# Optimization experiments

Hardware: AMD Instinct MI355X
Metric: run time of the kernel (lower is better)

## Reference

```python
import jax, jax.numpy as jnp
import numpy as np

B, N, D, H = 16, 256, 128, 8
HD = D // H
PAIR_DIMS = [64, 64, 64]
EPS = 1e-8


def _pairwise_lv_fts(x):
    # x: [B, 4, N] four-vectors (px, py, pz, E); returns [B, N, N, 4] = (lnkt, lnz, lndelta, lnm2)
    px, py, pz, e = x[:, 0], x[:, 1], x[:, 2], x[:, 3]
    pt = jnp.sqrt(jnp.clip(px ** 2 + py ** 2, EPS))          # [B, N]
    rap = 0.5 * jnp.log1p(2.0 * pz / jnp.clip(e - pz, 1e-20))
    phi = jnp.arctan2(py, px)
    d_rap = rap[:, :, None] - rap[:, None, :]                 # [B, N, N]
    d_phi = (phi[:, :, None] - phi[:, None, :] + np.pi) % (2.0 * np.pi) - np.pi
    delta = jnp.sqrt(d_rap ** 2 + d_phi ** 2)
    lndelta = jnp.log(jnp.clip(delta, EPS))
    ptmin = jnp.minimum(pt[:, :, None], pt[:, None, :])
    lnkt = jnp.log(jnp.clip(ptmin * delta, EPS))
    lnz = jnp.log(jnp.clip(ptmin / jnp.clip(pt[:, :, None] + pt[:, None, :], EPS), EPS))
    es = e[:, :, None] + e[:, None, :]
    pxs = px[:, :, None] + px[:, None, :]
    pys = py[:, :, None] + py[:, None, :]
    pzs = pz[:, :, None] + pz[:, None, :]
    lnm2 = jnp.log(jnp.clip(es ** 2 - pxs ** 2 - pys ** 2 - pzs ** 2, EPS))
    return jnp.stack([lnkt, lnz, lndelta, lnm2], axis=-1)


def setup_inputs() -> dict:
    key = jax.random.key(0)
    ks = jax.random.split(key, 12)
    p3 = jax.random.normal(ks[0], (B, 3, N), jnp.float32)
    e = jnp.sqrt((p3 ** 2).sum(1, keepdims=True)
                 + jnp.abs(jax.random.normal(ks[1], (B, 1, N), jnp.float32)) ** 2 + 0.1)
    x_pf = jnp.concatenate([p3, e], axis=1)                   # physical four-vectors [B,4,N]
    x_feat = jax.random.normal(ks[2], (B, N, D), jnp.float32) * 0.02
    dims = [4] + PAIR_DIMS + [H]
    pw = {}
    for i in range(4):
        pw[f"pair_w{i}"] = jax.random.normal(ks[3 + i], (dims[i], dims[i + 1]), jnp.float32) / np.sqrt(dims[i])
        pw[f"pair_b{i}"] = jnp.zeros((dims[i + 1],), jnp.float32)
    proj = {n: jax.random.normal(k, (D, D), jnp.float32) / np.sqrt(D)
            for n, k in zip(["wq", "wk", "wv", "wo"], jax.random.split(ks[7], 4))}
    bias = {n: jnp.zeros((D,), jnp.float32) for n in ["bq", "bk", "bv", "bo"]}
    return dict(x_pf=x_pf, x_feat=x_feat, **pw, **proj, **bias)


def reference(x_pf, x_feat, pair_w0, pair_b0, pair_w1, pair_b1, pair_w2, pair_b2,
              pair_w3, pair_b3, wq, wk, wv, wo, bq, bk, bv, bo):
    # pairwise Lorentz-invariant features -> dense attention bias
    u = _pairwise_lv_fts(x_pf)                                # [B, N, N, 4]
    for w, b in ((pair_w0, pair_b0), (pair_w1, pair_b1), (pair_w2, pair_b2)):
        u = jax.nn.gelu(u @ w + b)
    attn_bias = jnp.transpose(u @ pair_w3 + pair_b3, (0, 3, 1, 2))  # [B, H, N, N]
    # multi-head attention with pairwise bias
    q = (x_feat @ wq + bq).reshape(B, N, H, HD)
    k = (x_feat @ wk + bk).reshape(B, N, H, HD)
    v = (x_feat @ wv + bv).reshape(B, N, H, HD)
    scores = jnp.einsum("bihd,bjhd->bhij", q, k) / np.sqrt(HD) + attn_bias
    attn = jax.nn.softmax(scores, axis=-1)
    out = jnp.einsum("bhij,bjhd->bihd", attn, v).reshape(B, N, D)
    return out @ wo + bo                                      # [B, N, D]
```

## Files before the change

kernel.cpp:

```cpp
#include <hip/hip_runtime.h>
#include <hip/hip_bf16.h>
#include <math.h>

#define B_ 16
#define N_ 256
#define D_ 128
#define H_ 8
#define HD_ 16
#define EPS_ 1e-8f
#define PI_F 3.14159265358979323846f
#define TWO_PI_F 6.28318530717958647692f
#define INV_TWO_PI_F 0.15915494309189533577f
#define L2E_F 1.4426950408889634f

#define OFF_PT   0
#define OFF_RAP  4096
#define OFF_PHI  8192
#define OFF_PX   12288
#define OFF_PY   16384
#define OFF_PZ   20480
#define OFF_E    24576
#define OFF_Q    28672
#define OFF_BIAS (28672 + 3*524288)
#define OFF_AO   (OFF_BIAS + 8388608)
#define OFF_WPACK (OFF_AO + 524288)

#define UA0  0
#define UA1H 2048
#define UA1L 6144
#define UA2H 10240
#define UA2L 14336
#define UA3H 18432
#define UA3L 19456
#define UQKV 20480

typedef _Float16 f16x8 __attribute__((ext_vector_type(8)));
typedef _Float16 f16x4 __attribute__((ext_vector_type(4)));
typedef _Float16 f16x2 __attribute__((ext_vector_type(2)));
typedef __attribute__((ext_vector_type(4))) float f4;
typedef __attribute__((ext_vector_type(4))) unsigned int u4;

__device__ __forceinline__ unsigned pkh2(float a, float b) {
    f16x2 v = { (_Float16)a, (_Float16)b };
    return __builtin_bit_cast(unsigned, v);
}
__device__ __forceinline__ float f16res(float x) {
    return x - (float)(_Float16)x;
}

__device__ __forceinline__ float gelu_f(float x) {
    float y2 = x * fmaf(0.10294337f, x * x, 2.3022079f);
    float e = __builtin_amdgcn_exp2f(-y2);
    return x * __builtin_amdgcn_rcpf(1.0f + e);
}


__global__ __launch_bounds__(256) void k_prep(
    const float* __restrict__ w0, const float* __restrict__ w1,
    const float* __restrict__ w2, const float* __restrict__ w3,
    const float* __restrict__ wq, const float* __restrict__ wk,
    const float* __restrict__ wv, const float* __restrict__ wo,
    const float* __restrict__ x_pf,
    _Float16* __restrict__ wp, float* __restrict__ ws) {
    if (blockIdx.x >= 64) {
        int idx = (blockIdx.x - 64) * 256 + threadIdx.x;
        int b = idx >> 8, n = idx & 255;
        const float* base = x_pf + (size_t)b * 4 * N_;
        float px = base[0 * N_ + n];
        float py = base[1 * N_ + n];
        float pz = base[2 * N_ + n];
        float e  = base[3 * N_ + n];
        float pt  = sqrtf(fmaxf(px * px + py * py, EPS_));
        float rap = 0.5f * log1pf(2.0f * pz / fmaxf(e - pz, 1e-20f));
        float phi = atan2f(py, px);
        ws[OFF_PT  + idx] = pt;
        ws[OFF_RAP + idx] = rap;
        ws[OFF_PHI + idx] = phi;
        ws[OFF_PX  + idx] = px;
        ws[OFF_PY  + idx] = py;
        ws[OFF_PZ  + idx] = pz;
        ws[OFF_E   + idx] = e;
        return;
    }
    int id0 = blockIdx.x * 256 + threadIdx.x;
    const int gs = 64 * 256;
    for (int e = id0; e < 2048; e += gs) {
        int fi = e >> 3, j = e & 7;
        int mt = fi >> 6, lane = fi & 63;
        int q = lane >> 4, ln = lane & 15;
        int m = mt * 16 + ln;
        _Float16 v = (_Float16)0.0f;
        if (q == 0) v = (j < 4) ? (_Float16)w0[j * 64 + m]
                                : (_Float16)f16res(w0[(j - 4) * 64 + m]);
        else if (q == 1) v = (j < 4) ? (_Float16)w0[j * 64 + m] : (_Float16)0.0f;
        wp[UA0 + e] = v;
    }
    for (int e = id0; e < 4096; e += gs) {
        int fi = e >> 3, j = e & 7;
        int mt = fi >> 7, ks = (fi >> 6) & 1, lane = fi & 63;
        int q = lane >> 4;
        int m = mt * 16 + (lane & 15);
        int k = (2 * (j >> 2) + ks) * 16 + q * 4 + (j & 3);
        float x1 = w1[k * 64 + m];
        wp[UA1H + e] = (_Float16)x1;
        wp[UA1L + e] = (_Float16)f16res(x1);
        float x2 = w2[k * 64 + m];
        wp[UA2H + e] = (_Float16)x2;
        wp[UA2L + e] = (_Float16)f16res(x2);
    }
    for (int e = id0; e < 1024; e += gs) {
        int fi = e >> 3, j = e & 7;
        int ks = fi >> 6, lane = fi & 63;
        int q = lane >> 4;
        int m = lane & 15;
        int k = (2 * (j >> 2) + ks) * 16 + q * 4 + (j & 3);
        float x = (m < 8) ? w3[k * 8 + m] : 0.0f;
        wp[UA3H + e] = (_Float16)x;
        wp[UA3L + e] = (_Float16)f16res(x);
    }
    const float* mats[4] = { wq, wk, wv, wo };
#pragma unroll 1
    for (int mi = 0; mi < 4; ++mi) {
        const float* W = mats[mi];
        _Float16* dst = wp + UQKV + mi * 32768;
        for (int e = id0; e < 16384; e += gs) {
            int fi = e >> 3, j = e & 7;
            int mt = fi >> 8, ks = (fi >> 6) & 3, lane = fi & 63;
            int k = ks * 32 + ((lane >> 4) << 3) + j;
            int o = mt * 16 + (lane & 15);
            float x = W[k * 128 + o];
            dst[e] = (_Float16)x;
            dst[16384 + e] = (_Float16)f16res(x);
        }
    }
}

__device__ __forceinline__ void epi_frag(const f4 (&acc)[4][4], const float* __restrict__ bg,
                                         int q, u4 (&Bu)[4][2]) {
#pragma unroll
    for (int mt = 0; mt < 4; ++mt) {
        f4 bv = *(const f4*)&bg[mt * 16 + q * 4];
        int ks = mt & 1, hi = (mt >> 1) * 2;
#pragma unroll
        for (int nt = 0; nt < 4; ++nt) {
            float g0 = gelu_f(acc[mt][nt][0] + bv[0]);
            float g1 = gelu_f(acc[mt][nt][1] + bv[1]);
            float g2 = gelu_f(acc[mt][nt][2] + bv[2]);
            float g3 = gelu_f(acc[mt][nt][3] + bv[3]);
            Bu[nt][ks][hi]     = pkh2(g0, g1);
            Bu[nt][ks][hi + 1] = pkh2(g2, g3);
        }
    }
}

__device__ __forceinline__ void mid_layer(f4 (&acc)[4][4],
                                          const _Float16* __restrict__ wh,
                                          const _Float16* __restrict__ wl,
                                          int lane, const u4 (&Bu)[4][2]) {
    const f4 zero4 = { 0.f, 0.f, 0.f, 0.f };
#pragma unroll
    for (int mt = 0; mt < 4; ++mt) {
        f16x8 ah0 = *(const f16x8*)&wh[((mt * 2 + 0) * 64 + lane) * 8];
        f16x8 ah1 = *(const f16x8*)&wh[((mt * 2 + 1) * 64 + lane) * 8];
        f16x8 al0 = *(const f16x8*)&wl[((mt * 2 + 0) * 64 + lane) * 8];
        f16x8 al1 = *(const f16x8*)&wl[((mt * 2 + 1) * 64 + lane) * 8];
#pragma unroll
        for (int nt = 0; nt < 4; ++nt) {
            f16x8 b0 = __builtin_bit_cast(f16x8, Bu[nt][0]);
            f16x8 b1 = __builtin_bit_cast(f16x8, Bu[nt][1]);
            f4 c = zero4;
            c = __builtin_amdgcn_mfma_f32_16x16x32_f16(ah0, b0, c, 0, 0, 0);
            c = __builtin_amdgcn_mfma_f32_16x16x32_f16(al0, b0, c, 0, 0, 0);
            c = __builtin_amdgcn_mfma_f32_16x16x32_f16(ah1, b1, c, 0, 0, 0);
            c = __builtin_amdgcn_mfma_f32_16x16x32_f16(al1, b1, c, 0, 0, 0);
            acc[mt][nt] = c;
        }
    }
}

__device__ __forceinline__ void mfma_core64x16(
    const float* __restrict__ xrow, const _Float16* __restrict__ wpm,
    int mtbase, const float* __restrict__ biasv, int lane, f4 (&cc)[4]) {
    int q = lane >> 4;
    const f4 zero4 = { 0.f, 0.f, 0.f, 0.f };
    f16x8 Bh[4], Bl[4];
#pragma unroll
    for (int ks = 0; ks < 4; ++ks) {
        const float* p = xrow + ks * 32 + q * 8;
        float4 xa = ((const float4*)p)[0];
        float4 xb = ((const float4*)p)[1];
        u4 hu = { pkh2(xa.x, xa.y), pkh2(xa.z, xa.w), pkh2(xb.x, xb.y), pkh2(xb.z, xb.w) };
        u4 lu = { pkh2(f16res(xa.x), f16res(xa.y)), pkh2(f16res(xa.z), f16res(xa.w)),
                  pkh2(f16res(xb.x), f16res(xb.y)), pkh2(f16res(xb.z), f16res(xb.w)) };
        Bh[ks] = __builtin_bit_cast(f16x8, hu);
        Bl[ks] = __builtin_bit_cast(f16x8, lu);
    }
#pragma unroll
    for (int mtl = 0; mtl < 4; ++mtl) {
        int mt = mtbase + mtl;
        f4 c = zero4;
#pragma unroll
        for (int ks = 0; ks < 4; ++ks) {
            const _Float16* fa = wpm + ((size_t)((mt * 4 + ks) * 64 + lane)) * 8;
            f16x8 ah = *(const f16x8*)fa;
            f16x8 al = *(const f16x8*)(fa + 16384);
            c = __builtin_amdgcn_mfma_f32_16x16x32_f16(ah, Bh[ks], c, 0, 0, 0);
            c = __builtin_amdgcn_mfma_f32_16x16x32_f16(ah, Bl[ks], c, 0, 0, 0);
            c = __builtin_amdgcn_mfma_f32_16x16x32_f16(al, Bh[ks], c, 0, 0, 0);
        }
        f4 bv = *(const f4*)&biasv[mtl * 16 + q * 4];
        cc[mtl] = c + bv;
    }
}

__global__ __launch_bounds__(256, 4) void k_pair_qkv(
    const float* __restrict__ ws, const _Float16* __restrict__ wp,
    const float* __restrict__ b0g, const float* __restrict__ b1g,
    const float* __restrict__ b2g, const float* __restrict__ b3g,
    float* __restrict__ bias_out,
    const float* __restrict__ xf,
    const float* __restrict__ bqv, const float* __restrict__ bkv, const float* __restrict__ bvv,
    _Float16* __restrict__ qh, _Float16* __restrict__ kh,
    _Float16* __restrict__ kl, _Float16* __restrict__ vh) {
    int tid = threadIdx.x;
    int lane = tid & 63;
    int ln = lane & 15, q = lane >> 4;

    if (blockIdx.x < 384) {
        int wid = blockIdx.x * 4 + (tid >> 6);
        int og = wid % 6, tg = wid / 6;
        int mi = og >> 1, ch = og & 1;
        const _Float16* wpm = wp + UQKV + mi * 32768;
        const float* bias = (mi == 0) ? bqv : ((mi == 1) ? bkv : bvv);
        size_t tok = (size_t)(tg * 16 + ln);
        f4 cc[4];
        mfma_core64x16(xf + tok * 128, wpm, ch * 4, bias + ch * 64, lane, cc);
        _Float16* hout = (mi == 0) ? qh : ((mi == 1) ? kh : vh);
        int b = (int)(tok >> 8), tl = (int)(tok & 255);
#pragma unroll
        for (int mtl = 0; mtl < 4; ++mtl) {
            int head = ch * 4 + mtl;
            size_t off = ((size_t)((b * 8 + head) * 256 + tl)) * 16 + q * 4;
            f16x4 hv;
#pragma unroll
            for (int r = 0; r < 4; ++r) hv[r] = (_Float16)cc[mtl][r];
            *(f16x4*)&hout[off] = hv;
            if (mi == 1) {
                f16x4 lv;
#pragma unroll
                for (int r = 0; r < 4; ++r) lv[r] = (_Float16)(cc[mtl][r] - (float)hv[r]);
                *(f16x4*)&kl[off] = lv;
            }
        }
        return;
    }

    int w2 = (blockIdx.x - 384) * 4 + (tid >> 6);
    int b = w2 / 640;
    int w = w2 - b * 640;
    int it, rr, nj;
    if (w < 256)      { it = 0; rr = w;       nj = 4; }
    else if (w < 448) { it = 1; rr = w - 256; nj = 3; }
    else if (w < 576) { it = 2; rr = w - 448; nj = 2; }
    else              { it = 3; rr = w - 576; nj = 1; }
    int i  = it * 64 + rr / nj;
    int jt = it + rr % nj;
    int j0 = jt * 64;
    int row = (b << 8) + i;

    unsigned FH01, FH23, FL01, FL23;
    {
        int ib = row;
        int jb = (b << 8) + j0 + lane;
        float pt_i = ws[OFF_PT + ib],  rap_i = ws[OFF_RAP + ib], phi_i = ws[OFF_PHI + ib];
        float px_i = ws[OFF_PX + ib],  py_i  = ws[OFF_PY  + ib];
        float pz_i = ws[OFF_PZ + ib],  e_i   = ws[OFF_E   + ib];
        float pt_j = ws[OFF_PT + jb],  rap_j = ws[OFF_RAP + jb], phi_j = ws[OFF_PHI + jb];
        float px_j = ws[OFF_PX + jb],  py_j  = ws[OFF_PY  + jb];
        float pz_j = ws[OFF_PZ + jb],  e_j   = ws[OFF_E   + jb];

        float drap = rap_i - rap_j;
        float xw = phi_i - phi_j + PI_F;
        float mw = xw - TWO_PI_F * floorf(xw * INV_TWO_PI_F);
        float dphi = mw - PI_F;
        float delta = sqrtf(drap * drap + dphi * dphi);
        float f2 = __logf(fmaxf(delta, EPS_));
        float ptmin = fminf(pt_i, pt_j);
        float f0 = __logf(fmaxf(ptmin * delta, EPS_));
        float f1 = __logf(fmaxf(ptmin / fmaxf(pt_i + pt_j, EPS_), EPS_));
        float es = e_i + e_j, pxs = px_i + px_j, pys = py_i + py_j, pzs = pz_i + pz_j;
        float f3 = __logf(fmaxf(es * es - pxs * pxs - pys * pys - pzs * pzs, EPS_));

        FH01 = pkh2(f0, f1);
        FH23 = pkh2(f2, f3);
        FL01 = pkh2(f16res(f0), f16res(f1));
        FL23 = pkh2(f16res(f2), f16res(f3));
    }

    f4 acc[4][4];
    const f4 zero4 = { 0.f, 0.f, 0.f, 0.f };

    {
        f16x8 a0[4];
#pragma unroll
        for (int mt = 0; mt < 4; ++mt)
            a0[mt] = *(const f16x8*)&wp[UA0 + (mt * 64 + lane) * 8];
#pragma unroll
        for (int nt = 0; nt < 4; ++nt) {
            int src = nt * 16 + ln;
            unsigned h01 = (unsigned)__shfl((int)FH01, src);
            unsigned h23 = (unsigned)__shfl((int)FH23, src);
            unsigned l01 = (unsigned)__shfl((int)FL01, src);
            unsigned l23 = (unsigned)__shfl((int)FL23, src);
            u4 bu;
            bu[0] = (q == 0) ? h01 : ((q == 1) ? l01 : 0u);
            bu[1] = (q == 0) ? h23 : ((q == 1) ? l23 : 0u);
            bu[2] = (q == 0) ? h01 : 0u;
            bu[3] = (q == 0) ? h23 : 0u;
            f16x8 bf = __builtin_bit_cast(f16x8, bu);
#pragma unroll
            for (int mt = 0; mt < 4; ++mt)
                acc[mt][nt] = __builtin_amdgcn_mfma_f32_16x16x32_f16(a0[mt], bf, zero4, 0, 0, 0);
        }
    }

    u4 Bu[4][2];
    epi_frag(acc, b0g, q, Bu);
    mid_layer(acc, wp + UA1H, wp + UA1L, lane, Bu);
    epi_frag(acc, b1g, q, Bu);
    mid_layer(acc, wp + UA2H, wp + UA2L, lane, Bu);
    epi_frag(acc, b2g, q, Bu);

    {
        f16x8 a3h0 = *(const f16x8*)&wp[UA3H + (0 * 64 + lane) * 8];
        f16x8 a3h1 = *(const f16x8*)&wp[UA3H + (1 * 64 + lane) * 8];
        f16x8 a3l0 = *(const f16x8*)&wp[UA3L + (0 * 64 + lane) * 8];
        f16x8 a3l1 = *(const f16x8*)&wp[UA3L + (1 * 64 + lane) * 8];
        f4 acc3[4];
#pragma unroll
        for (int nt = 0; nt < 4; ++nt) {
            f16x8 b0 = __builtin_bit_cast(f16x8, Bu[nt][0]);
            f16x8 b1 = __builtin_bit_cast(f16x8, Bu[nt][1]);
            f4 c = zero4;
            c = __builtin_amdgcn_mfma_f32_16x16x32_f16(a3h0, b0, c, 0, 0, 0);
            c = __builtin_amdgcn_mfma_f32_16x16x32_f16(a3l0, b0, c, 0, 0, 0);
            c = __builtin_amdgcn_mfma_f32_16x16x32_f16(a3h1, b1, c, 0, 0, 0);
            c = __builtin_amdgcn_mfma_f32_16x16x32_f16(a3l1, b1, c, 0, 0, 0);
            acc3[nt] = c;
        }
        if (q < 2) {
            f4 b3v = *(const f4*)&b3g[q * 4];
#pragma unroll
            for (int nt = 0; nt < 4; ++nt) {
                int jc = j0 + nt * 16 + ln;
#pragma unroll
                for (int r = 0; r < 4; ++r) {
                    int out = q * 4 + r;
                    bias_out[(((size_t)(b * H_ + out)) * N_ + i) * N_ + jc] = acc3[nt][r] + b3v[r];
                }
            }
        }
    }
}

#define SVT 264
__global__ __launch_bounds__(256) void k_attn(
    const float* __restrict__ ws,
    const _Float16* __restrict__ qh, const _Float16* __restrict__ kh,
    const _Float16* __restrict__ kl, const _Float16* __restrict__ vh,
    float* __restrict__ wso) {
    __shared__ __align__(16) _Float16 Vt[16 * SVT];
    __shared__ float cm[4 * 16];
    __shared__ float cl[4 * 16];
    __shared__ float cO[4][16][20];
    int tid = threadIdx.x;
    int blk = blockIdx.x;
    int it = blk & 15;
    int bh = blk >> 4;
    int b = bh >> 3;

    {
        const _Float16* vr = vh + ((size_t)(bh * 256) + tid) * 16;
        f16x8 v0 = *(const f16x8*)vr;
        f16x8 v1 = *(const f16x8*)(vr + 8);
#pragma unroll
        for (int d = 0; d < 8; ++d) {
            Vt[d * SVT + tid] = v0[d];
            Vt[(8 + d) * SVT + tid] = v1[d];
        }
    }
    __syncthreads();

    int lane = tid & 63, w = tid >> 6;
    int ln = lane & 15, q = lane >> 4;
    int i0 = it * 16;
    const f4 zero4 = { 0.f, 0.f, 0.f, 0.f };

    f16x8 Bq = *(const f16x8*)&qh[((size_t)(bh * 256) + i0 + ln) * 16 + (q & 1) * 8];

    f4 accs[4];
    const _Float16* kbase = (q < 2 ? kh : kl) + ((size_t)(bh * 256)) * 16 + (q & 1) * 8;
    bool lower = (w < (it >> 2));
    const float* bb = ws + OFF_BIAS + ((size_t)(bh * 256 + i0 + ln)) * 256 + w * 64 + q * 4;
    const float* tbb = ws + OFF_BIAS + ((size_t)bh) * 65536 + (size_t)(w * 64 + q * 4) * 256 + (i0 + ln);
#pragma unroll
    for (int mt = 0; mt < 4; ++mt) {
        int jl = w * 64 + mt * 16 + ln;
        f16x8 Ak = *(const f16x8*)&kbase[(size_t)jl * 16];
        f4 s = __builtin_amdgcn_mfma_f32_16x16x32_f16(Ak, Bq, zero4, 0, 0, 0);
        f4 bias4;
        if (lower) {
            const float* tb = tbb + (size_t)(mt * 16) * 256;
            bias4[0] = tb[0];
            bias4[1] = tb[256];
            bias4[2] = tb[512];
            bias4[3] = tb[768];
        } else {
            bias4 = *(const f4*)&bb[mt * 16];
        }
#pragma unroll
        for (int r = 0; r < 4; ++r) s[r] = fmaf(s[r], 0.25f, bias4[r]);
        accs[mt] = s;
    }

    float mx = accs[0][0];
#pragma unroll
    for (int mt = 0; mt < 4; ++mt)
#pragma unroll
        for (int r = 0; r < 4; ++r) mx = fmaxf(mx, accs[mt][r]);
    mx = fmaxf(mx, __shfl_xor(mx, 16));
    mx = fmaxf(mx, __shfl_xor(mx, 32));
    float nms = -mx * L2E_F;
    float l = 0.0f;
#pragma unroll
    for (int mt = 0; mt < 4; ++mt) {
#pragma unroll
        for (int r = 0; r < 4; ++r) {
            float p = __builtin_amdgcn_exp2f(fmaf(accs[mt][r], L2E_F, nms));
            accs[mt][r] = p;
            l += p;
        }
    }
    l += __shfl_xor(l, 16);
    l += __shfl_xor(l, 32);

    f4 o = zero4;
#pragma unroll
    for (int ks = 0; ks < 2; ++ks) {
        u4 bp = { pkh2(accs[2 * ks][0], accs[2 * ks][1]),
                  pkh2(accs[2 * ks][2], accs[2 * ks][3]),
                  pkh2(accs[2 * ks + 1][0], accs[2 * ks + 1][1]),
                  pkh2(accs[2 * ks + 1][2], accs[2 * ks + 1][3]) };
        int vb = ln * SVT + w * 64 + 32 * ks + 4 * q;
        f16x4 lo4 = *(const f16x4*)&Vt[vb];
        f16x4 hi4 = *(const f16x4*)&Vt[vb + 16];
        f16x8 av;
        av[0] = lo4[0]; av[1] = lo4[1]; av[2] = lo4[2]; av[3] = lo4[3];
        av[4] = hi4[0]; av[5] = hi4[1]; av[6] = hi4[2]; av[7] = hi4[3];
        o = __builtin_amdgcn_mfma_f32_16x16x32_f16(av, __builtin_bit_cast(f16x8, bp), o, 0, 0, 0);
    }

    if (q == 0) { cm[w * 16 + ln] = mx; cl[w * 16 + ln] = l; }
#pragma unroll
    for (int r = 0; r < 4; ++r) cO[w][q * 4 + r][ln] = o[r];
    __syncthreads();

    if (w == 0) {
        float m0 = cm[ln], m1 = cm[16 + ln], m2 = cm[32 + ln], m3 = cm[48 + ln];
        float M = fmaxf(fmaxf(m0, m1), fmaxf(m2, m3));
        float s0 = __builtin_amdgcn_exp2f((m0 - M) * L2E_F);
        float s1 = __builtin_amdgcn_exp2f((m1 - M) * L2E_F);
        float s2 = __builtin_amdgcn_exp2f((m2 - M) * L2E_F);
        float s3 = __builtin_amdgcn_exp2f((m3 - M) * L2E_F);
        float L = s0 * cl[ln] + s1 * cl[16 + ln] + s2 * cl[32 + ln] + s3 * cl[48 + ln];
        float inv = __builtin_amdgcn_rcpf(L);
        f4 res;
#pragma unroll
        for (int r = 0; r < 4; ++r) {
            int d = q * 4 + r;
            float v = s0 * cO[0][d][ln] + s1 * cO[1][d][ln]
                    + s2 * cO[2][d][ln] + s3 * cO[3][d][ln];
            res[r] = v * inv;
        }
        int h = bh & 7;
        *(f4*)(wso + OFF_AO + ((size_t)(b * 256 + i0 + ln)) * 128 + h * 16 + q * 4) = res;
    }
}

__global__ __launch_bounds__(256) void k_out(
    const float* __restrict__ ws, const _Float16* __restrict__ wp,
    const float* __restrict__ bo, float* __restrict__ out) {
    int tid = threadIdx.x;
    int lane = tid & 63, ln = lane & 15, q = lane >> 4;
    int wid = blockIdx.x * 4 + (tid >> 6);
    int og = wid & 1, tg = wid >> 1;
    const _Float16* wpm = wp + UQKV + 3 * 32768;
    size_t tok = (size_t)(tg * 16 + ln);
    f4 cc[4];
    mfma_core64x16(ws + OFF_AO + tok * 128, wpm, og * 4, bo + og * 64, lane, cc);
#pragma unroll
    for (int mtl = 0; mtl < 4; ++mtl)
        *(f4*)(out + tok * 128 + og * 64 + mtl * 16 + q * 4) = cc[mtl];
}

extern "C" void kernel_launch(void* const* d_in, const int* in_sizes, int n_in,
                              void* d_out, int out_size, void* d_ws, size_t ws_size,
                              hipStream_t stream) {
    const float* x_pf   = (const float*)d_in[0];
    const float* x_feat = (const float*)d_in[1];
    const float* w0 = (const float*)d_in[2];
    const float* b0 = (const float*)d_in[3];
    const float* w1 = (const float*)d_in[4];
    const float* b1 = (const float*)d_in[5];
    const float* w2 = (const float*)d_in[6];
    const float* b2 = (const float*)d_in[7];
    const float* w3 = (const float*)d_in[8];
    const float* b3 = (const float*)d_in[9];
    const float* wq = (const float*)d_in[10];
    const float* wk = (const float*)d_in[11];
    const float* wv = (const float*)d_in[12];
    const float* wo = (const float*)d_in[13];
    const float* bq = (const float*)d_in[14];
    const float* bk = (const float*)d_in[15];
    const float* bv = (const float*)d_in[16];
    const float* bo = (const float*)d_in[17];
    float* ws  = (float*)d_ws;
    float* out = (float*)d_out;
    _Float16* wpack = (_Float16*)(ws + OFF_WPACK);
    _Float16* qh = (_Float16*)(ws + OFF_Q);
    _Float16* kh = qh + 524288;
    _Float16* kl = kh + 524288;
    _Float16* vh = kl + 524288;

    hipLaunchKernelGGL(k_prep, dim3(80), dim3(256), 0, stream,
                       w0, w1, w2, w3, wq, wk, wv, wo, x_pf, wpack, ws);
    hipLaunchKernelGGL(k_pair_qkv, dim3(384 + 2560), dim3(256), 0, stream,
                       ws, wpack, b0, b1, b2, b3, ws + OFF_BIAS,
                       x_feat, bq, bk, bv, qh, kh, kl, vh);
    hipLaunchKernelGGL(k_attn, dim3(2048), dim3(256), 0, stream, ws, qh, kh, kl, vh, ws);
    hipLaunchKernelGGL(k_out, dim3(128), dim3(256), 0, stream, ws, wpack, bo, out);
}
```

Before: 158.2 us.

## Use packed RTZ f16 conversions, raise pair kernel occupancy, shrink output blocks

Replaces the scalar round-to-nearest f16 conversions with the packed cvt_pkrtz instruction in several places: the hi/lo split packing, the GELU epilogue, the Q/K/V stores and the softmax-probability packing. It also reuses the packed hi values when computing the lo residuals. The pair/QKV kernel's launch-bounds occupancy hint goes from 4 to 6, which limits registers per thread and may cause spills. The output projection now runs 512 single-wave blocks instead of 128 four-wave blocks. RTZ rounding changes numerics slightly; the hi/lo residual scheme mostly compensates for this.

```diff
diff --git a/kernel.cpp b/kernel.cpp
--- a/kernel.cpp
+++ b/kernel.cpp
@@ -46,6 +46,12 @@
 }
 __device__ __forceinline__ float f16res(float x) {
     return x - (float)(_Float16)x;
+}
+__device__ __forceinline__ f16x2 pkrtz(float a, float b) {
+    return __builtin_bit_cast(f16x2, __builtin_amdgcn_cvt_pkrtz(a, b));
+}
+__device__ __forceinline__ unsigned pkrtz_u(float a, float b) {
+    return __builtin_bit_cast(unsigned, __builtin_amdgcn_cvt_pkrtz(a, b));
 }
 
 __device__ __forceinline__ float gelu_f(float x) {
@@ -147,8 +153,8 @@
             float g1 = gelu_f(acc[mt][nt][1] + bv[1]);
             float g2 = gelu_f(acc[mt][nt][2] + bv[2]);
             float g3 = gelu_f(acc[mt][nt][3] + bv[3]);
-            Bu[nt][ks][hi]     = pkh2(g0, g1);
-            Bu[nt][ks][hi + 1] = pkh2(g2, g3);
+            Bu[nt][ks][hi]     = pkrtz_u(g0, g1);
+            Bu[nt][ks][hi + 1] = pkrtz_u(g2, g3);
         }
     }
 }
@@ -189,9 +195,14 @@
         const float* p = xrow + ks * 32 + q * 8;
         float4 xa = ((const float4*)p)[0];
         float4 xb = ((const float4*)p)[1];
-        u4 hu = { pkh2(xa.x, xa.y), pkh2(xa.z, xa.w), pkh2(xb.x, xb.y), pkh2(xb.z, xb.w) };
-        u4 lu = { pkh2(f16res(xa.x), f16res(xa.y)), pkh2(f16res(xa.z), f16res(xa.w)),
-                  pkh2(f16res(xb.x), f16res(xb.y)), pkh2(f16res(xb.z), f16res(xb.w)) };
+        f16x2 h0 = pkrtz(xa.x, xa.y), h1 = pkrtz(xa.z, xa.w);
+        f16x2 h2 = pkrtz(xb.x, xb.y), h3 = pkrtz(xb.z, xb.w);
+        u4 hu = { __builtin_bit_cast(unsigned, h0), __builtin_bit_cast(unsigned, h1),
+                  __builtin_bit_cast(unsigned, h2), __builtin_bit_cast(unsigned, h3) };
+        u4 lu = { pkrtz_u(xa.x - (float)h0[0], xa.y - (float)h0[1]),
+                  pkrtz_u(xa.z - (float)h1[0], xa.w - (float)h1[1]),
+                  pkrtz_u(xb.x - (float)h2[0], xb.y - (float)h2[1]),
+                  pkrtz_u(xb.z - (float)h3[0], xb.w - (float)h3[1]) };
         Bh[ks] = __builtin_bit_cast(f16x8, hu);
         Bl[ks] = __builtin_bit_cast(f16x8, lu);
     }
@@ -213,7 +224,7 @@
     }
 }
 
-__global__ __launch_bounds__(256, 4) void k_pair_qkv(
+__global__ __launch_bounds__(256, 6) void k_pair_qkv(
     const float* __restrict__ ws, const _Float16* __restrict__ wp,
     const float* __restrict__ b0g, const float* __restrict__ b1g,
     const float* __restrict__ b2g, const float* __restrict__ b3g,
@@ -241,14 +252,16 @@
         for (int mtl = 0; mtl < 4; ++mtl) {
             int head = ch * 4 + mtl;
             size_t off = ((size_t)((b * 8 + head) * 256 + tl)) * 16 + q * 4;
+            f16x2 h0 = pkrtz(cc[mtl][0], cc[mtl][1]);
+            f16x2 h1 = pkrtz(cc[mtl][2], cc[mtl][3]);
             f16x4 hv;
-#pragma unroll
-            for (int r = 0; r < 4; ++r) hv[r] = (_Float16)cc[mtl][r];
+            hv[0] = h0[0]; hv[1] = h0[1]; hv[2] = h1[0]; hv[3] = h1[1];
             *(f16x4*)&hout[off] = hv;
             if (mi == 1) {
+                f16x2 l0 = pkrtz(cc[mtl][0] - (float)h0[0], cc[mtl][1] - (float)h0[1]);
+                f16x2 l1 = pkrtz(cc[mtl][2] - (float)h1[0], cc[mtl][3] - (float)h1[1]);
                 f16x4 lv;
-#pragma unroll
-                for (int r = 0; r < 4; ++r) lv[r] = (_Float16)(cc[mtl][r] - (float)hv[r]);
+                lv[0] = l0[0]; lv[1] = l0[1]; lv[2] = l1[0]; lv[3] = l1[1];
                 *(f16x4*)&kl[off] = lv;
             }
         }
@@ -291,10 +304,11 @@
         float es = e_i + e_j, pxs = px_i + px_j, pys = py_i + py_j, pzs = pz_i + pz_j;
         float f3 = __logf(fmaxf(es * es - pxs * pxs - pys * pys - pzs * pzs, EPS_));
 
-        FH01 = pkh2(f0, f1);
-        FH23 = pkh2(f2, f3);
-        FL01 = pkh2(f16res(f0), f16res(f1));
-        FL23 = pkh2(f16res(f2), f16res(f3));
+        f16x2 h01 = pkrtz(f0, f1), h23 = pkrtz(f2, f3);
+        FH01 = __builtin_bit_cast(unsigned, h01);
+        FH23 = __builtin_bit_cast(unsigned, h23);
+        FL01 = pkrtz_u(f0 - (float)h01[0], f1 - (float)h01[1]);
+        FL23 = pkrtz_u(f2 - (float)h23[0], f3 - (float)h23[1]);
     }
 
     f4 acc[4][4];
@@ -447,10 +461,10 @@
     f4 o = zero4;
 #pragma unroll
     for (int ks = 0; ks < 2; ++ks) {
-        u4 bp = { pkh2(accs[2 * ks][0], accs[2 * ks][1]),
-                  pkh2(accs[2 * ks][2], accs[2 * ks][3]),
-                  pkh2(accs[2 * ks + 1][0], accs[2 * ks + 1][1]),
-                  pkh2(accs[2 * ks + 1][2], accs[2 * ks + 1][3]) };
+        u4 bp = { pkrtz_u(accs[2 * ks][0], accs[2 * ks][1]),
+                  pkrtz_u(accs[2 * ks][2], accs[2 * ks][3]),
+                  pkrtz_u(accs[2 * ks + 1][0], accs[2 * ks + 1][1]),
+                  pkrtz_u(accs[2 * ks + 1][2], accs[2 * ks + 1][3]) };
         int vb = ln * SVT + w * 64 + 32 * ks + 4 * q;
         f16x4 lo4 = *(const f16x4*)&Vt[vb];
         f16x4 hi4 = *(const f16x4*)&Vt[vb + 16];
@@ -487,12 +501,11 @@
     }
 }
 
-__global__ __launch_bounds__(256) void k_out(
+__global__ __launch_bounds__(64) void k_out(
     const float* __restrict__ ws, const _Float16* __restrict__ wp,
     const float* __restrict__ bo, float* __restrict__ out) {
-    int tid = threadIdx.x;
-    int lane = tid & 63, ln = lane & 15, q = lane >> 4;
-    int wid = blockIdx.x * 4 + (tid >> 6);
+    int lane = threadIdx.x & 63, ln = lane & 15, q = lane >> 4;
+    int wid = blockIdx.x;
     int og = wid & 1, tg = wid >> 1;
     const _Float16* wpm = wp + UQKV + 3 * 32768;
     size_t tok = (size_t)(tg * 16 + ln);
@@ -538,5 +551,5 @@
                        ws, wpack, b0, b1, b2, b3, ws + OFF_BIAS,
                        x_feat, bq, bk, bv, qh, kh, kl, vh);
     hipLaunchKernelGGL(k_attn, dim3(2048), dim3(256), 0, stream, ws, qh, kh, kl, vh, ws);
-    hipLaunchKernelGGL(k_out, dim3(128), dim3(256), 0, stream, ws, wpack, bo, out);
-}
+    hipLaunchKernelGGL(k_out, dim3(512), dim3(64), 0, stream, ws, wpack, bo, out);
+}
```

Result: slower. 207.6 us (+31.2%).
